# Optimization experiments

Measured on AMD Instinct MI355X. Metric: run time of the kernel, lower is better.

The kernel has to match this reference:

```python
import jax, jax.numpy as jnp
import numpy as np

B, N, D, H = 4, 2048, 1024, 64

def setup_inputs() -> dict:
    key = jax.random.key(0)
    ks = jax.random.split(key, 7)
    s = D ** -0.5  # torch Linear default init scale ~ U(-1/sqrt(fan_in), ...); scale randn similarly
    return {
        "x":  jax.random.normal(ks[0], (B, N, D), dtype=jnp.float32),
        "Wq": jax.random.normal(ks[1], (D, H), dtype=jnp.float32) * s,
        "bq": jax.random.normal(ks[2], (H,), dtype=jnp.float32) * s,
        "Wk": jax.random.normal(ks[3], (D, H), dtype=jnp.float32) * s,
        "bk": jax.random.normal(ks[4], (H,), dtype=jnp.float32) * s,
        "Wv": jax.random.normal(ks[5], (D, H), dtype=jnp.float32) * s,
        "bv": jax.random.normal(ks[6], (H,), dtype=jnp.float32) * s,
    }

def reference(x, Wq, bq, Wk, bk, Wv, bv):
    head_size = Wq.shape[1]
    q = x @ Wq + bq          # [B, N, H]
    k = x @ Wk + bk          # [B, N, H]
    v = x @ Wv + bv          # [B, N, H]
    scores = jnp.einsum("bid,bjd->bij", q, k)        # [B, N, N]
    # faithful to torch: keep upper triangle (col >= row), then mask exact zeros to -inf
    scores = jnp.triu(scores)
    scores = jnp.where(scores == 0, -jnp.inf, scores)
    attn = jax.nn.softmax(scores * (head_size ** -0.5), axis=-1)  # [B, N, N]
    # out = (V^T @ attn)^T  ==  attn^T @ V
    out = jnp.einsum("bji,bjh->bih", attn, v)         # [B, N, H]
    return out
```

## Files before the change

kernel.cpp:

```cpp
#include <hip/hip_runtime.h>

constexpr int kN = 2048;
constexpr int kD = 1024;

typedef __attribute__((ext_vector_type(8))) short bf16x8;
typedef __attribute__((ext_vector_type(4))) short bf16x4;
typedef __attribute__((ext_vector_type(4))) float f32x4;

#define MFMA(a, b, c) __builtin_amdgcn_mfma_f32_16x16x32_bf16(a, b, c, 0, 0, 0)

constexpr float kExpC = 0.18033688011112042f;
#define EXP8(sv) __builtin_amdgcn_exp2f((sv) * kExpC)

__device__ __forceinline__ short f2bf(float f) {
    unsigned u = __float_as_uint(f);
    u += 0x7fff + ((u >> 16) & 1);
    return (short)(u >> 16);
}

__device__ __forceinline__ void g2l(void* lds, const void* g, int nbytes, int t) {
    int lane = t & 63, w = t >> 6;
    for (int base = w * 1024; base < nbytes; base += 4096) {
        if (base + lane * 16 < nbytes) {
            __builtin_amdgcn_global_load_lds(
                (const __attribute__((address_space(1))) void*)((const char*)g + base + lane * 16),
                (__attribute__((address_space(3))) void*)((char*)lds + base),
                16, 0, 0);
        }
    }
}

__global__ __launch_bounds__(256) void prep_kernel(
        const float* __restrict__ Wq, const float* __restrict__ Wk,
        const float* __restrict__ Wv, const float* __restrict__ bq,
        const float* __restrict__ bk, const float* __restrict__ bv,
        short* __restrict__ Wt, float* __restrict__ bcat)
{
    int tid = blockIdx.x * 256 + threadIdx.x;
    int stride = gridDim.x * 256;
    for (int e = tid; e < 16 * 12 * 2 * 512; e += stride) {
        int kc = e / 12288;
        int rem = e - kc * 12288;
        int nt = rem >> 10;
        int r2 = rem & 1023;
        int f = r2 >> 9;
        int r3 = r2 & 511;
        int q8 = r3 >> 7;
        int l15 = (r3 >> 3) & 15;
        int el = r3 & 7;
        int n = nt * 16 + l15;
        int d = kc * 64 + f * 32 + q8 * 8 + el;
        float wv = (n < 64) ? Wq[d * 64 + n]
                 : (n < 128) ? Wk[d * 64 + (n - 64)]
                 : Wv[d * 64 + (n - 128)];
        Wt[e] = f2bf(wv);
    }
    if (tid < 192)
        bcat[tid] = (tid < 64) ? bq[tid] : (tid < 128) ? bk[tid - 64] : bv[tid - 128];
}

constexpr int XP = 1032;

__global__ __launch_bounds__(256) void qkv_kernel(
        const float* __restrict__ x, const short* __restrict__ Wt,
        const float* __restrict__ bcat,
        short* __restrict__ gq, short* __restrict__ gk, short* __restrict__ vt)
{
    __shared__ __align__(16) short xs[16 * XP];
    const int t = threadIdx.x;
    const int w = t >> 6, lane = t & 63, l15 = lane & 15, q8 = lane >> 4;
    const int m0 = blockIdx.x * 16;

    {
        int row = t >> 4, c4 = (t & 15) * 4;
        const float* xr = x + (size_t)(m0 + row) * kD;
        #pragma unroll
        for (int cc = 0; cc < 16; ++cc) {
            float4 xv = *(const float4*)&xr[cc * 64 + c4];
            bf16x4 pk = {f2bf(xv.x), f2bf(xv.y), f2bf(xv.z), f2bf(xv.w)};
            *(bf16x4*)&xs[row * XP + cc * 64 + c4] = pk;
        }
    }
    __syncthreads();

    f32x4 acc[3];
    #pragma unroll
    for (int ct = 0; ct < 3; ++ct) acc[ct] = (f32x4){0.f, 0.f, 0.f, 0.f};

    #pragma unroll 4
    for (int kc = 0; kc < 16; ++kc) {
        bf16x8 a0 = *(const bf16x8*)&xs[l15 * XP + kc * 64 + q8 * 8];
        bf16x8 a1 = *(const bf16x8*)&xs[l15 * XP + kc * 64 + 32 + q8 * 8];
        #pragma unroll
        for (int ct = 0; ct < 3; ++ct) {
            int nt = w * 3 + ct;
            const short* bp = Wt + ((size_t)(kc * 12 + nt) * 2) * 512 + lane * 8;
            bf16x8 b0 = *(const bf16x8*)bp;
            bf16x8 b1 = *(const bf16x8*)(bp + 512);
            acc[ct] = MFMA(a0, b0, acc[ct]);
            acc[ct] = MFMA(a1, b1, acc[ct]);
        }
    }

    const int bz = m0 >> 11;
    const int jt = (m0 & 2047) >> 6;
    const int jb = m0 & 63;
    #pragma unroll
    for (int ct = 0; ct < 3; ++ct) {
        int nb2 = w * 48 + ct * 16;
        int n = nb2 + l15;
        float bias = bcat[n];
        if (nb2 < 64) {
            #pragma unroll
            for (int r = 0; r < 4; ++r)
                gq[(size_t)(m0 + q8 * 4 + r) * 72 + n] = f2bf(acc[ct][r] + bias);
        } else if (nb2 < 128) {
            #pragma unroll
            for (int r = 0; r < 4; ++r)
                gk[(size_t)(m0 + q8 * 4 + r) * 72 + (n - 64)] = f2bf(acc[ct][r] + bias);
        } else {
            int h = n - 128;
            bf16x4 pk = {f2bf(acc[ct][0] + bias), f2bf(acc[ct][1] + bias),
                         f2bf(acc[ct][2] + bias), f2bf(acc[ct][3] + bias)};
            *(bf16x4*)&vt[((size_t)((bz * 32 + jt) * 64 + h)) * 72 + jb + q8 * 4] = pk;
        }
    }
}

__global__ __launch_bounds__(256) void stats_kernel(
        const short* __restrict__ gq, const short* __restrict__ gk,
        float* __restrict__ l2)
{
    __shared__ __align__(16) short ksm[2][64 * 72];
    const int t = threadIdx.x;
    const int w = t >> 6, lane = t & 63, l15 = lane & 15, q8 = lane >> 4;
    const int b = blockIdx.x;
    const int ic = b & 3, bz = (b >> 2) & 3, jt = b >> 4;
    const int j0 = jt * 64;
    const int ilo = ic * 512, ihi = ilo + 512;
    const int istart = (j0 > ilo) ? j0 : ilo;
    const int count = (istart < ihi) ? ((ihi - istart) >> 6) : 0;

    float lloc[4] = {0.f, 0.f, 0.f, 0.f};

    if (count > 0) {
        const short* qp = gq + (size_t)(bz * kN + j0 + 16 * w + l15) * 72 + q8 * 8;
        bf16x8 a0 = *(const bf16x8*)qp;
        bf16x8 a1 = *(const bf16x8*)(qp + 32);
        g2l(ksm[0], gk + (size_t)(bz * kN + istart) * 72, 64 * 144, t);
        __syncthreads();

        for (int idx = 0; idx < count; ++idx) {
            const int cur = idx & 1;
            if (idx + 1 < count)
                g2l(ksm[cur ^ 1],
                    gk + (size_t)(bz * kN + istart + (idx + 1) * 64) * 72, 64 * 144, t);
            const int i0 = istart + idx * 64;
            #pragma unroll
            for (int it = 0; it < 4; ++it) {
                int irow = it * 16 + l15;
                bf16x8 b0 = *(const bf16x8*)&ksm[cur][irow * 72 + q8 * 8];
                bf16x8 b1 = *(const bf16x8*)&ksm[cur][irow * 72 + 32 + q8 * 8];
                f32x4 s = (f32x4){0.f, 0.f, 0.f, 0.f};
                s = MFMA(a0, b0, s);
                s = MFMA(a1, b1, s);
                int ig = i0 + it * 16 + l15;
                if (i0 + it * 16 >= j0 + 16 * w + 15) {
                    #pragma unroll
                    for (int r = 0; r < 4; ++r) {
                        float sv = s[r];
                        lloc[r] += (sv != 0.0f) ? EXP8(sv) : 0.0f;
                    }
                } else {
                    #pragma unroll
                    for (int r = 0; r < 4; ++r) {
                        int jg = j0 + 16 * w + q8 * 4 + r;
                        float sv = s[r];
                        lloc[r] += ((ig >= jg) && (sv != 0.0f)) ? EXP8(sv) : 0.0f;
                    }
                }
            }
            __syncthreads();
        }
    }
    #pragma unroll
    for (int off = 1; off < 16; off <<= 1)
        #pragma unroll
        for (int r = 0; r < 4; ++r)
            lloc[r] += __shfl_xor(lloc[r], off);
    if (l15 == 0) {
        #pragma unroll
        for (int r = 0; r < 4; ++r)
            l2[ic * 8192 + bz * kN + j0 + 16 * w + q8 * 4 + r] = lloc[r];
    }
}

__global__ __launch_bounds__(256) void out_kernel(
        const short* __restrict__ gq, const short* __restrict__ gk,
        const short* __restrict__ vt, const float* __restrict__ l2,
        float* __restrict__ part)
{
    __shared__ __align__(16) short vsm[2][64 * 72];
    __shared__ __align__(16) short psm[64 * 72];
    __shared__ __align__(16) float rsm[512];
    const int t = threadIdx.x;
    const int w = t >> 6, lane = t & 63, l15 = lane & 15, q8 = lane >> 4;
    const int b = blockIdx.x;
    const int jc = b & 3, bz = (b >> 2) & 3, it = b >> 4;
    const int i0 = it * 64;
    const int jlo = jc * 512;
    const int jhi = (jlo + 512 < i0 + 64) ? (jlo + 512) : (i0 + 64);
    const int count = (jlo < jhi) ? ((jhi - jlo) >> 6) : 0;

    #pragma unroll
    for (int jj = t; jj < 512; jj += 256) {
        int j = bz * kN + jlo + jj;
        float l = l2[j] + l2[8192 + j] + l2[16384 + j] + l2[24576 + j];
        rsm[jj] = (l > 0.f) ? 1.0f / l : 0.0f;
    }

    f32x4 oacc[4];
    #pragma unroll
    for (int i = 0; i < 4; ++i) oacc[i] = (f32x4){0.f, 0.f, 0.f, 0.f};

    if (count > 0) {
        bf16x8 kb0[4], kb1[4];
        #pragma unroll
        for (int itile = 0; itile < 4; ++itile) {
            const short* kp = gk + (size_t)(bz * kN + i0 + itile * 16 + l15) * 72 + q8 * 8;
            kb0[itile] = *(const bf16x8*)kp;
            kb1[itile] = *(const bf16x8*)(kp + 32);
        }
        g2l(vsm[0], vt + (size_t)((bz * 32 + (jlo >> 6)) * 64) * 72, 64 * 144, t);
        const short* qp = gq + (size_t)(bz * kN + jlo + 16 * w + l15) * 72 + q8 * 8;
        bf16x8 qa0 = *(const bf16x8*)qp;
        bf16x8 qa1 = *(const bf16x8*)(qp + 32);
        __syncthreads();

        for (int idx = 0; idx < count; ++idx) {
            const int cur = idx & 1, nb = cur ^ 1;
            const int j0s = jlo + idx * 64;
            const bool more = (idx + 1 < count);
            bf16x8 qn0, qn1;
            if (more) {
                g2l(vsm[nb], vt + (size_t)((bz * 32 + ((j0s + 64) >> 6)) * 64) * 72,
                    64 * 144, t);
                const short* qn =
                    gq + (size_t)(bz * kN + j0s + 64 + 16 * w + l15) * 72 + q8 * 8;
                qn0 = *(const bf16x8*)qn;
                qn1 = *(const bf16x8*)(qn + 32);
            }
            f32x4 rl4 = *(const f32x4*)&rsm[(j0s - jlo) + 16 * w + q8 * 4];

            #pragma unroll
            for (int itile = 0; itile < 4; ++itile) {
                f32x4 s = (f32x4){0.f, 0.f, 0.f, 0.f};
                s = MFMA(qa0, kb0[itile], s);
                s = MFMA(qa1, kb1[itile], s);
                int ig = i0 + itile * 16 + l15;
                bf16x4 pk;
                if (i0 + itile * 16 >= j0s + 16 * w + 15) {
                    #pragma unroll
                    for (int r = 0; r < 4; ++r) {
                        float sv = s[r];
                        float p = (sv != 0.0f) ? EXP8(sv) * rl4[r] : 0.0f;
                        pk[r] = f2bf(p);
                    }
                } else {
                    #pragma unroll
                    for (int r = 0; r < 4; ++r) {
                        int jg = j0s + 16 * w + q8 * 4 + r;
                        float sv = s[r];
                        float p = ((ig >= jg) && (sv != 0.0f))
                                  ? EXP8(sv) * rl4[r] : 0.0f;
                        pk[r] = f2bf(p);
                    }
                }
                *(bf16x4*)&psm[(itile * 16 + l15) * 72 + 16 * w + q8 * 4] = pk;
            }
            __syncthreads();

            bf16x8 pa0 = *(const bf16x8*)&psm[(16 * w + l15) * 72 + q8 * 8];
            bf16x8 pa1 = *(const bf16x8*)&psm[(16 * w + l15) * 72 + 32 + q8 * 8];
            #pragma unroll
            for (int ht = 0; ht < 4; ++ht) {
                int vrow = ht * 16 + l15;
                bf16x8 vb0 = *(const bf16x8*)&vsm[cur][vrow * 72 + q8 * 8];
                bf16x8 vb1 = *(const bf16x8*)&vsm[cur][vrow * 72 + 32 + q8 * 8];
                oacc[ht] = MFMA(pa0, vb0, oacc[ht]);
                oacc[ht] = MFMA(pa1, vb1, oacc[ht]);
            }
            __syncthreads();
            if (more) { qa0 = qn0; qa1 = qn1; }
        }
    }
    size_t base = ((size_t)(jc * 4 + bz) * kN + i0) * 64;
    #pragma unroll
    for (int ht = 0; ht < 4; ++ht)
        #pragma unroll
        for (int r = 0; r < 4; ++r)
            part[base + (size_t)(16 * w + q8 * 4 + r) * 64 + ht * 16 + l15] = oacc[ht][r];
}

__global__ __launch_bounds__(256) void reduce_kernel(
        const float* __restrict__ part, float* __restrict__ out)
{
    int idx = blockIdx.x * 256 + threadIdx.x;
    const float4* p = (const float4*)part;
    float4 a = p[idx];
    float4 b = p[idx + 131072];
    float4 c = p[idx + 262144];
    float4 d = p[idx + 393216];
    float4 r;
    r.x = a.x + b.x + c.x + d.x;
    r.y = a.y + b.y + c.y + d.y;
    r.z = a.z + b.z + c.z + d.z;
    r.w = a.w + b.w + c.w + d.w;
    ((float4*)out)[idx] = r;
}

extern "C" void kernel_launch(void* const* d_in, const int* in_sizes, int n_in,
                              void* d_out, int out_size, void* d_ws, size_t ws_size,
                              hipStream_t stream)
{
    const float* x  = (const float*)d_in[0];
    const float* Wq = (const float*)d_in[1];
    const float* bq = (const float*)d_in[2];
    const float* Wk = (const float*)d_in[3];
    const float* bk = (const float*)d_in[4];
    const float* Wv = (const float*)d_in[5];
    const float* bv = (const float*)d_in[6];
    float* out = (float*)d_out;

    char* base = (char*)d_ws;
    short* Wt   = (short*)(base);
    float* bcat = (float*)(base + 393216);
    short* gq   = (short*)(base + 394240);
    short* gk   = (short*)(base + 1573888);
    short* vt   = (short*)(base + 2753536);
    float* l2   = (float*)(base + 3933184);
    float* part = (float*)(base + 4064256);

    prep_kernel<<<256, 256, 0, stream>>>(Wq, Wk, Wv, bq, bk, bv, Wt, bcat);
    qkv_kernel<<<512, 256, 0, stream>>>(x, Wt, bcat, gq, gk, vt);
    stats_kernel<<<512, 256, 0, stream>>>(gq, gk, l2);
    out_kernel<<<512, 256, 0, stream>>>(gq, gk, vt, l2, part);
    reduce_kernel<<<512, 256, 0, stream>>>(part, out);
}
```

Before: 122.6 us.

## Drop LDS staging for K/V, split stats over 8 chunks, skip empty blocks

The stats and out kernels stop double-buffering K and V tiles through LDS with async global-to-LDS loads. Each lane now reads its MFMA operands straight from global memory into registers, which removes barriers and LDS traffic. The stats kernel splits the key range into 8 chunks of 256 instead of 4 of 512, doubling the grid for more parallelism on the triangular workload. The out kernel exits early for fully masked blocks, and the reduce kernel sums only the partial buffers that can be non-zero. The risk is redundant global/L2 reads, since the four waves each load the same K/V rows, and less latency hiding without the prefetch.

```diff
diff --git a/kernel.cpp b/kernel.cpp
--- a/kernel.cpp
+++ b/kernel.cpp
@@ -16,18 +16,6 @@
     unsigned u = __float_as_uint(f);
     u += 0x7fff + ((u >> 16) & 1);
     return (short)(u >> 16);
-}
-
-__device__ __forceinline__ void g2l(void* lds, const void* g, int nbytes, int t) {
-    int lane = t & 63, w = t >> 6;
-    for (int base = w * 1024; base < nbytes; base += 4096) {
-        if (base + lane * 16 < nbytes) {
-            __builtin_amdgcn_global_load_lds(
-                (const __attribute__((address_space(1))) void*)((const char*)g + base + lane * 16),
-                (__attribute__((address_space(3))) void*)((char*)lds + base),
-                16, 0, 0);
-        }
-    }
 }
 
 __global__ __launch_bounds__(256) void prep_kernel(
@@ -131,13 +119,12 @@
         const short* __restrict__ gq, const short* __restrict__ gk,
         float* __restrict__ l2)
 {
-    __shared__ __align__(16) short ksm[2][64 * 72];
     const int t = threadIdx.x;
     const int w = t >> 6, lane = t & 63, l15 = lane & 15, q8 = lane >> 4;
     const int b = blockIdx.x;
-    const int ic = b & 3, bz = (b >> 2) & 3, jt = b >> 4;
+    const int ic = b & 7, bz = (b >> 3) & 3, jt = b >> 5;
     const int j0 = jt * 64;
-    const int ilo = ic * 512, ihi = ilo + 512;
+    const int ilo = ic * 256, ihi = ilo + 256;
     const int istart = (j0 > ilo) ? j0 : ilo;
     const int count = (istart < ihi) ? ((ihi - istart) >> 6) : 0;
 
@@ -147,20 +134,14 @@
         const short* qp = gq + (size_t)(bz * kN + j0 + 16 * w + l15) * 72 + q8 * 8;
         bf16x8 a0 = *(const bf16x8*)qp;
         bf16x8 a1 = *(const bf16x8*)(qp + 32);
-        g2l(ksm[0], gk + (size_t)(bz * kN + istart) * 72, 64 * 144, t);
-        __syncthreads();
 
         for (int idx = 0; idx < count; ++idx) {
-            const int cur = idx & 1;
-            if (idx + 1 < count)
-                g2l(ksm[cur ^ 1],
-                    gk + (size_t)(bz * kN + istart + (idx + 1) * 64) * 72, 64 * 144, t);
             const int i0 = istart + idx * 64;
+            const short* kp = gk + (size_t)(bz * kN + i0 + l15) * 72 + q8 * 8;
             #pragma unroll
             for (int it = 0; it < 4; ++it) {
-                int irow = it * 16 + l15;
-                bf16x8 b0 = *(const bf16x8*)&ksm[cur][irow * 72 + q8 * 8];
-                bf16x8 b1 = *(const bf16x8*)&ksm[cur][irow * 72 + 32 + q8 * 8];
+                bf16x8 b0 = *(const bf16x8*)(kp + (size_t)(it * 16) * 72);
+                bf16x8 b1 = *(const bf16x8*)(kp + (size_t)(it * 16) * 72 + 32);
                 f32x4 s = (f32x4){0.f, 0.f, 0.f, 0.f};
                 s = MFMA(a0, b0, s);
                 s = MFMA(a1, b1, s);
@@ -180,7 +161,6 @@
                     }
                 }
             }
-            __syncthreads();
         }
     }
     #pragma unroll
@@ -200,7 +180,6 @@
         const short* __restrict__ vt, const float* __restrict__ l2,
         float* __restrict__ part)
 {
-    __shared__ __align__(16) short vsm[2][64 * 72];
     __shared__ __align__(16) short psm[64 * 72];
     __shared__ __align__(16) float rsm[512];
     const int t = threadIdx.x;
@@ -211,11 +190,13 @@
     const int jlo = jc * 512;
     const int jhi = (jlo + 512 < i0 + 64) ? (jlo + 512) : (i0 + 64);
     const int count = (jlo < jhi) ? ((jhi - jlo) >> 6) : 0;
-
-    #pragma unroll
+    if (count == 0) return;
+
     for (int jj = t; jj < 512; jj += 256) {
         int j = bz * kN + jlo + jj;
-        float l = l2[j] + l2[8192 + j] + l2[16384 + j] + l2[24576 + j];
+        float l = 0.f;
+        #pragma unroll
+        for (int c = 0; c < 8; ++c) l += l2[c * 8192 + j];
         rsm[jj] = (l > 0.f) ? 1.0f / l : 0.0f;
     }
 
@@ -223,77 +204,77 @@
     #pragma unroll
     for (int i = 0; i < 4; ++i) oacc[i] = (f32x4){0.f, 0.f, 0.f, 0.f};
 
-    if (count > 0) {
-        bf16x8 kb0[4], kb1[4];
+    bf16x8 kb0[4], kb1[4];
+    #pragma unroll
+    for (int itile = 0; itile < 4; ++itile) {
+        const short* kp = gk + (size_t)(bz * kN + i0 + itile * 16 + l15) * 72 + q8 * 8;
+        kb0[itile] = *(const bf16x8*)kp;
+        kb1[itile] = *(const bf16x8*)(kp + 32);
+    }
+    const short* qp = gq + (size_t)(bz * kN + jlo + 16 * w + l15) * 72 + q8 * 8;
+    bf16x8 qa0 = *(const bf16x8*)qp;
+    bf16x8 qa1 = *(const bf16x8*)(qp + 32);
+    __syncthreads();
+
+    for (int idx = 0; idx < count; ++idx) {
+        const int j0s = jlo + idx * 64;
+        const bool more = (idx + 1 < count);
+
+        const short* vp = vt + (size_t)((bz * 32 + (j0s >> 6)) * 64 + l15) * 72 + q8 * 8;
+        bf16x8 vb0[4], vb1[4];
+        #pragma unroll
+        for (int ht = 0; ht < 4; ++ht) {
+            vb0[ht] = *(const bf16x8*)(vp + (size_t)(ht * 16) * 72);
+            vb1[ht] = *(const bf16x8*)(vp + (size_t)(ht * 16) * 72 + 32);
+        }
+        bf16x8 qn0, qn1;
+        if (more) {
+            const short* qn =
+                gq + (size_t)(bz * kN + j0s + 64 + 16 * w + l15) * 72 + q8 * 8;
+            qn0 = *(const bf16x8*)qn;
+            qn1 = *(const bf16x8*)(qn + 32);
+        }
+        f32x4 rl4 = *(const f32x4*)&rsm[(j0s - jlo) + 16 * w + q8 * 4];
+
         #pragma unroll
         for (int itile = 0; itile < 4; ++itile) {
-            const short* kp = gk + (size_t)(bz * kN + i0 + itile * 16 + l15) * 72 + q8 * 8;
-            kb0[itile] = *(const bf16x8*)kp;
-            kb1[itile] = *(const bf16x8*)(kp + 32);
-        }
-        g2l(vsm[0], vt + (size_t)((bz * 32 + (jlo >> 6)) * 64) * 72, 64 * 144, t);
-        const short* qp = gq + (size_t)(bz * kN + jlo + 16 * w + l15) * 72 + q8 * 8;
-        bf16x8 qa0 = *(const bf16x8*)qp;
-        bf16x8 qa1 = *(const bf16x8*)(qp + 32);
+            f32x4 s = (f32x4){0.f, 0.f, 0.f, 0.f};
+            s = MFMA(qa0, kb0[itile], s);
+            s = MFMA(qa1, kb1[itile], s);
+            int ig = i0 + itile * 16 + l15;
+            bf16x4 pk;
+            if (i0 + itile * 16 >= j0s + 16 * w + 15) {
+                #pragma unroll
+                for (int r = 0; r < 4; ++r) {
+                    float sv = s[r];
+                    float p = (sv != 0.0f) ? EXP8(sv) * rl4[r] : 0.0f;
+                    pk[r] = f2bf(p);
+                }
+            } else {
+                #pragma unroll
+                for (int r = 0; r < 4; ++r) {
+                    int jg = j0s + 16 * w + q8 * 4 + r;
+                    float sv = s[r];
+                    float p = ((ig >= jg) && (sv != 0.0f))
+                              ? EXP8(sv) * rl4[r] : 0.0f;
+                    pk[r] = f2bf(p);
+                }
+            }
+            *(bf16x4*)&psm[(itile * 16 + l15) * 72 + 16 * w + q8 * 4] = pk;
+        }
         __syncthreads();
 
-        for (int idx = 0; idx < count; ++idx) {
-            const int cur = idx & 1, nb = cur ^ 1;
-            const int j0s = jlo + idx * 64;
-            const bool more = (idx + 1 < count);
-            bf16x8 qn0, qn1;
-            if (more) {
-                g2l(vsm[nb], vt + (size_t)((bz * 32 + ((j0s + 64) >> 6)) * 64) * 72,
-                    64 * 144, t);
-                const short* qn =
-                    gq + (size_t)(bz * kN + j0s + 64 + 16 * w + l15) * 72 + q8 * 8;
-                qn0 = *(const bf16x8*)qn;
-                qn1 = *(const bf16x8*)(qn + 32);
-            }
-            f32x4 rl4 = *(const f32x4*)&rsm[(j0s - jlo) + 16 * w + q8 * 4];
-
-            #pragma unroll
-            for (int itile = 0; itile < 4; ++itile) {
-                f32x4 s = (f32x4){0.f, 0.f, 0.f, 0.f};
-                s = MFMA(qa0, kb0[itile], s);
-                s = MFMA(qa1, kb1[itile], s);
-                int ig = i0 + itile * 16 + l15;
-                bf16x4 pk;
-                if (i0 + itile * 16 >= j0s + 16 * w + 15) {
-                    #pragma unroll
-                    for (int r = 0; r < 4; ++r) {
-                        float sv = s[r];
-                        float p = (sv != 0.0f) ? EXP8(sv) * rl4[r] : 0.0f;
-                        pk[r] = f2bf(p);
-                    }
-                } else {
-                    #pragma unroll
-                    for (int r = 0; r < 4; ++r) {
-                        int jg = j0s + 16 * w + q8 * 4 + r;
-                        float sv = s[r];
-                        float p = ((ig >= jg) && (sv != 0.0f))
-                                  ? EXP8(sv) * rl4[r] : 0.0f;
-                        pk[r] = f2bf(p);
-                    }
-                }
-                *(bf16x4*)&psm[(itile * 16 + l15) * 72 + 16 * w + q8 * 4] = pk;
-            }
-            __syncthreads();
-
-            bf16x8 pa0 = *(const bf16x8*)&psm[(16 * w + l15) * 72 + q8 * 8];
-            bf16x8 pa1 = *(const bf16x8*)&psm[(16 * w + l15) * 72 + 32 + q8 * 8];
-            #pragma unroll
-            for (int ht = 0; ht < 4; ++ht) {
-                int vrow = ht * 16 + l15;
-                bf16x8 vb0 = *(const bf16x8*)&vsm[cur][vrow * 72 + q8 * 8];
-                bf16x8 vb1 = *(const bf16x8*)&vsm[cur][vrow * 72 + 32 + q8 * 8];
-                oacc[ht] = MFMA(pa0, vb0, oacc[ht]);
-                oacc[ht] = MFMA(pa1, vb1, oacc[ht]);
-            }
-            __syncthreads();
-            if (more) { qa0 = qn0; qa1 = qn1; }
-        }
-    }
+        bf16x8 pa0 = *(const bf16x8*)&psm[(16 * w + l15) * 72 + q8 * 8];
+        bf16x8 pa1 = *(const bf16x8*)&psm[(16 * w + l15) * 72 + 32 + q8 * 8];
+        #pragma unroll
+        for (int ht = 0; ht < 4; ++ht) {
+            oacc[ht] = MFMA(pa0, vb0[ht], oacc[ht]);
+            oacc[ht] = MFMA(pa1, vb1[ht], oacc[ht]);
+        }
+        __syncthreads();
+        if (more) { qa0 = qn0; qa1 = qn1; }
+    }
+
     size_t base = ((size_t)(jc * 4 + bz) * kN + i0) * 64;
     #pragma unroll
     for (int ht = 0; ht < 4; ++ht)
@@ -306,16 +287,14 @@
         const float* __restrict__ part, float* __restrict__ out)
 {
     int idx = blockIdx.x * 256 + threadIdx.x;
+    int i = (idx >> 4) & 2047;
+    int nvalid = (i >> 9) + 1;
     const float4* p = (const float4*)part;
-    float4 a = p[idx];
-    float4 b = p[idx + 131072];
-    float4 c = p[idx + 262144];
-    float4 d = p[idx + 393216];
-    float4 r;
-    r.x = a.x + b.x + c.x + d.x;
-    r.y = a.y + b.y + c.y + d.y;
-    r.z = a.z + b.z + c.z + d.z;
-    r.w = a.w + b.w + c.w + d.w;
+    float4 r = p[idx];
+    for (int c = 1; c < nvalid; ++c) {
+        float4 v = p[idx + c * 131072];
+        r.x += v.x; r.y += v.y; r.z += v.z; r.w += v.w;
+    }
     ((float4*)out)[idx] = r;
 }
 
@@ -339,11 +318,11 @@
     short* gk   = (short*)(base + 1573888);
     short* vt   = (short*)(base + 2753536);
     float* l2   = (float*)(base + 3933184);
-    float* part = (float*)(base + 4064256);
+    float* part = (float*)(base + 4195328);
 
     prep_kernel<<<256, 256, 0, stream>>>(Wq, Wk, Wv, bq, bk, bv, Wt, bcat);
     qkv_kernel<<<512, 256, 0, stream>>>(x, Wt, bcat, gq, gk, vt);
-    stats_kernel<<<512, 256, 0, stream>>>(gq, gk, l2);
+    stats_kernel<<<1024, 256, 0, stream>>>(gq, gk, l2);
     out_kernel<<<512, 256, 0, stream>>>(gq, gk, vt, l2, part);
     reduce_kernel<<<512, 256, 0, stream>>>(part, out);
 }
```

New measurement: 125.4 us. 2.3% more time.
